# Optimization experiments

Measured on AMD Instinct MI355X. Metric: run time of the kernel, lower is better.

## Reference

```python
import jax, jax.numpy as jnp
import numpy as np

B, T, D, H = 256, 256, 384, 64  # batch, seq (BLOCK_SIZE), D_MODEL, HEAD_SIZE


def setup_inputs() -> dict:
    key = jax.random.key(0)
    k1, k2, k3, k4 = jax.random.split(key, 4)
    x = jax.random.normal(k1, (B, T, D), dtype=jnp.float32)
    # nn.Linear(D, H, bias=False): weight [H, D]; we store transposed [D, H] for x @ W
    Wq = jax.random.normal(k2, (D, H), dtype=jnp.float32) * (1.0 / np.sqrt(D))
    Wk = jax.random.normal(k3, (D, H), dtype=jnp.float32) * (1.0 / np.sqrt(D))
    Wv = jax.random.normal(k4, (D, H), dtype=jnp.float32) * (1.0 / np.sqrt(D))
    return {"x": x, "Wq": Wq, "Wk": Wk, "Wv": Wv}


def reference(x, Wq, Wk, Wv):
    # x: [B, T, D]
    q = x @ Wq  # [B, T, H]
    k = x @ Wk  # [B, T, H]
    v = x @ Wv  # [B, T, H]
    scale = 1.0 / jnp.sqrt(jnp.asarray(k.shape[-1], dtype=x.dtype))
    wei = jnp.einsum('bth,bsh->bts', q, k) * scale  # [B, T, T]
    causal = jnp.tril(jnp.ones((x.shape[1], x.shape[1]), dtype=bool))
    wei = jnp.where(causal, wei, -jnp.inf)
    wei = jax.nn.softmax(wei, axis=-1)
    # dropout is identity in eval mode (deterministic reference)
    out = jnp.einsum('bts,bsh->bth', wei, v)  # [B, T, H]
    return out
```

## Files before the change

### kernel.cpp

```cpp
#include <hip/hip_runtime.h>

#define BATCH 256
#define TT 256
#define DD 384
#define HH 64
#define SCALE 0.125f
#define SHIFT 14.0f

typedef __attribute__((ext_vector_type(8))) short short8;
typedef __attribute__((ext_vector_type(4))) float floatx4;

#define KS_STRIDE 72
#define QS_STRIDE 72
#define VT_STRIDE 264
#define PS_STRIDE 40

__device__ __forceinline__ unsigned short f2bf(float f) {
    unsigned int u = __float_as_uint(f);
    u += 0x7fffu + ((u >> 16) & 1u);
    return (unsigned short)(u >> 16);
}
__device__ __forceinline__ float bf2f(unsigned short u) {
    return __uint_as_float(((unsigned int)u) << 16);
}

__device__ __forceinline__ void gld_lds16(const float* g, float* ldst) {
    __builtin_amdgcn_global_load_lds(
        (__attribute__((address_space(1))) void*)(unsigned long long)(const void*)g,
        (__attribute__((address_space(3))) void*)(unsigned int)(unsigned long long)(void*)ldst,
        16, 0, 0);
}

__global__ void pack_w_kernel(const float* __restrict__ wq,
                              const float* __restrict__ wk,
                              const float* __restrict__ wv,
                              unsigned short* __restrict__ wf) {
    int idx = blockIdx.x * 256 + threadIdx.x;
    if (idx >= 3 * DD * HH) return;
    int j = idx & 7;
    int lane = (idx >> 3) & 63;
    int nt = (idx >> 9) & 3;
    int rem = idx >> 11;
    int mat = rem % 3;
    int ch = rem / 3;
    int l16 = lane & 15, q = lane >> 4;
    int h = 16 * nt + l16;
    int d = 32 * ch + 8 * q + j;
    const float* w = (mat == 0) ? wq : (mat == 1) ? wk : wv;
    wf[idx] = f2bf(w[d * HH + h]);
}

__device__ __forceinline__ short8 afrag(const float* xsbuf, int row, int quad) {
    int r7 = row & 7;
    float4 f0 = *(const float4*)(xsbuf + row * 32 + ((2 * quad) ^ r7) * 4);
    float4 f1 = *(const float4*)(xsbuf + row * 32 + ((2 * quad + 1) ^ r7) * 4);
    short8 a;
    a[0] = (short)f2bf(f0.x); a[1] = (short)f2bf(f0.y);
    a[2] = (short)f2bf(f0.z); a[3] = (short)f2bf(f0.w);
    a[4] = (short)f2bf(f1.x); a[5] = (short)f2bf(f1.y);
    a[6] = (short)f2bf(f1.z); a[7] = (short)f2bf(f1.w);
    return a;
}

__global__ __launch_bounds__(512, 2)
void fused_kernel(const float* __restrict__ x, const unsigned short* __restrict__ wfrag,
                  float* __restrict__ out) {
    __shared__ __align__(16) unsigned short Ks[TT * KS_STRIDE];
    __shared__ __align__(16) unsigned short Vt[HH * VT_STRIDE];
    __shared__ __align__(16) union StageU {
        float xs[2][TT * 32];
        struct {
            unsigned short q[TT * QS_STRIDE];
            unsigned short p[8][16 * PS_STRIDE];
        } s;
    } U;

    const int b = blockIdx.x;
    const int tid = threadIdx.x;
    const int wave = tid >> 6;
    const int lane = tid & 63;
    const int quad = lane >> 4;
    const int l16 = lane & 15;

    const float* xb = x + (size_t)b * TT * DD;

    floatx4 cq[2][4] = {};
    floatx4 ck[2][4] = {};
    floatx4 cv[2][4] = {};

    #define STAGE_X(buf_, kk_)                                                    \
        {                                                                         \
            _Pragma("unroll")                                                     \
            for (int rr = 0; rr < 4; ++rr) {                                      \
                int u = rr * 512 + wave * 64 + lane;                              \
                int row_ = u >> 3;                                                \
                int slot_ = (u & 7) ^ (row_ & 7);                                 \
                gld_lds16(xb + row_ * DD + (kk_) + slot_ * 4,                     \
                          U.xs[buf_] + (rr * 512 + wave * 64) * 4);               \
            }                                                                     \
        }

    short8 wf[12], wfn[12];
    #pragma unroll
    for (int i = 0; i < 12; ++i)
        wf[i] = *(const short8*)(wfrag + (size_t)i * 512 + lane * 8);
    STAGE_X(0, 0);

    for (int ch = 0; ch < 12; ++ch) {
        __syncthreads();
        if (ch + 1 < 12) {
            #pragma unroll
            for (int i = 0; i < 12; ++i)
                wfn[i] = *(const short8*)(wfrag + (size_t)((ch + 1) * 12 + i) * 512 + lane * 8);
            STAGE_X((ch + 1) & 1, (ch + 1) * 32);
        }
        const float* xsb = U.xs[ch & 1];
        short8 a0 = afrag(xsb, 32 * wave + l16, quad);
        short8 a1 = afrag(xsb, 32 * wave + 16 + l16, quad);
        #pragma unroll
        for (int nt = 0; nt < 4; ++nt) {
            cq[0][nt] = __builtin_amdgcn_mfma_f32_16x16x32_bf16(a0, wf[nt], cq[0][nt], 0, 0, 0);
            cq[1][nt] = __builtin_amdgcn_mfma_f32_16x16x32_bf16(a1, wf[nt], cq[1][nt], 0, 0, 0);
            ck[0][nt] = __builtin_amdgcn_mfma_f32_16x16x32_bf16(a0, wf[4 + nt], ck[0][nt], 0, 0, 0);
            ck[1][nt] = __builtin_amdgcn_mfma_f32_16x16x32_bf16(a1, wf[4 + nt], ck[1][nt], 0, 0, 0);
            cv[0][nt] = __builtin_amdgcn_mfma_f32_16x16x32_bf16(a0, wf[8 + nt], cv[0][nt], 0, 0, 0);
            cv[1][nt] = __builtin_amdgcn_mfma_f32_16x16x32_bf16(a1, wf[8 + nt], cv[1][nt], 0, 0, 0);
        }
        #pragma unroll
        for (int i = 0; i < 12; ++i) wf[i] = wfn[i];
    }

    __syncthreads();

    #pragma unroll
    for (int mi = 0; mi < 2; ++mi)
      #pragma unroll
      for (int nt = 0; nt < 4; ++nt)
        #pragma unroll
        for (int r = 0; r < 4; ++r) {
            int row = 32 * wave + 16 * mi + 4 * quad + r;
            int col = 16 * nt + l16;
            U.s.q[row * QS_STRIDE + col] = f2bf(cq[mi][nt][r]);
            Ks[row * KS_STRIDE + col] = f2bf(ck[mi][nt][r]);
            Vt[col * VT_STRIDE + row] = f2bf(cv[mi][nt][r]);
        }

    __syncthreads();

    floatx4 o[2][4] = {};
    float l_run[2][4] = {{0.f, 0.f, 0.f, 0.f}, {0.f, 0.f, 0.f, 0.f}};
    unsigned short* psw = U.s.p[wave];

    #pragma unroll
    for (int gi = 0; gi < 2; ++gi) {
        int g = gi ? (15 - wave) : wave;
        int gr0 = 16 * g;
        short8 aq0 = *(const short8*)(U.s.q + (gr0 + l16) * QS_STRIDE + quad * 8);
        short8 aq1 = *(const short8*)(U.s.q + (gr0 + l16) * QS_STRIDE + 32 + quad * 8);
        int clast = g >> 1;
        for (int c = 0; c <= clast; ++c) {
            floatx4 s[2] = {};
            #pragma unroll
            for (int ni = 0; ni < 2; ++ni) {
                const unsigned short* kbase =
                    Ks + (size_t)(32 * c + 16 * ni + l16) * KS_STRIDE + quad * 8;
                s[ni] = __builtin_amdgcn_mfma_f32_16x16x32_bf16(aq0, *(const short8*)(kbase), s[ni], 0, 0, 0);
                s[ni] = __builtin_amdgcn_mfma_f32_16x16x32_bf16(aq1, *(const short8*)(kbase + 32), s[ni], 0, 0, 0);
            }
            bool partial = (c == clast);
            #pragma unroll
            for (int r = 0; r < 4; ++r) {
                int row = gr0 + 4 * quad + r;
                float p0 = __expf(s[0][r] * SCALE - SHIFT);
                float p1 = __expf(s[1][r] * SCALE - SHIFT);
                if (partial) {
                    if (32 * c + l16 > row) p0 = 0.f;
                    if (32 * c + 16 + l16 > row) p1 = 0.f;
                }
                unsigned short b0 = f2bf(p0), b1 = f2bf(p1);
                l_run[gi][r] += bf2f(b0) + bf2f(b1);
                psw[(4 * quad + r) * PS_STRIDE + l16] = b0;
                psw[(4 * quad + r) * PS_STRIDE + 16 + l16] = b1;
            }
            short8 ap = *(const short8*)(psw + l16 * PS_STRIDE + quad * 8);
            #pragma unroll
            for (int nt = 0; nt < 4; ++nt) {
                short8 bv = *(const short8*)(Vt + (size_t)(16 * nt + l16) * VT_STRIDE + 32 * c + quad * 8);
                o[gi][nt] = __builtin_amdgcn_mfma_f32_16x16x32_bf16(ap, bv, o[gi][nt], 0, 0, 0);
            }
        }
    }

    float* outb = out + (size_t)b * TT * HH;
    #pragma unroll
    for (int gi = 0; gi < 2; ++gi) {
        int g = gi ? (15 - wave) : wave;
        #pragma unroll
        for (int r = 0; r < 4; ++r) {
            float l = l_run[gi][r];
            l += __shfl_xor(l, 1);
            l += __shfl_xor(l, 2);
            l += __shfl_xor(l, 4);
            l += __shfl_xor(l, 8);
            l_run[gi][r] = l;
        }
        #pragma unroll
        for (int nt = 0; nt < 4; ++nt)
          #pragma unroll
          for (int r = 0; r < 4; ++r) {
            int row = 16 * g + 4 * quad + r;
            outb[(size_t)row * HH + 16 * nt + l16] = o[gi][nt][r] / l_run[gi][r];
          }
    }
}

extern "C" void kernel_launch(void* const* d_in, const int* in_sizes, int n_in,
                              void* d_out, int out_size, void* d_ws, size_t ws_size,
                              hipStream_t stream) {
    const float* x  = (const float*)d_in[0];
    const float* wq = (const float*)d_in[1];
    const float* wk = (const float*)d_in[2];
    const float* wv = (const float*)d_in[3];
    unsigned short* wf = (unsigned short*)d_ws;
    float* o = (float*)d_out;

    pack_w_kernel<<<(3 * DD * HH + 255) / 256, 256, 0, stream>>>(wq, wk, wv, wf);
    fused_kernel<<<BATCH, 512, 0, stream>>>(x, wf, o);
}
```

Baseline: 168.8 us.

## Stage packed weights in LDS once and stream x directly into registers

All bf16 weight fragments (144 KB) are copied into LDS once at block start, replacing the per-chunk global reloads of weights. The x chunks are now loaded straight from global into registers with a register double-buffer, instead of going through LDS staging with a barrier every chunk. This removes 12 barriers and repeated weight traffic from the projection loop. The cost is more LDS per block (the union now holds 144 KB), which may limit occupancy to one block per CU despite launch_bounds(512,2). It also uses uncoalesced row-strided x loads from global memory.

```diff
diff --git a/kernel.cpp b/kernel.cpp
--- a/kernel.cpp
+++ b/kernel.cpp
@@ -14,6 +14,7 @@
 #define QS_STRIDE 72
 #define VT_STRIDE 264
 #define PS_STRIDE 40
+#define WELEMS (3 * DD * HH)
 
 __device__ __forceinline__ unsigned short f2bf(float f) {
     unsigned int u = __float_as_uint(f);
@@ -24,11 +25,20 @@
     return __uint_as_float(((unsigned int)u) << 16);
 }
 
-__device__ __forceinline__ void gld_lds16(const float* g, float* ldst) {
+__device__ __forceinline__ void gld_lds16(const void* g, void* ldst) {
     __builtin_amdgcn_global_load_lds(
-        (__attribute__((address_space(1))) void*)(unsigned long long)(const void*)g,
-        (__attribute__((address_space(3))) void*)(unsigned int)(unsigned long long)(void*)ldst,
+        (__attribute__((address_space(1))) void*)(unsigned long long)g,
+        (__attribute__((address_space(3))) void*)(unsigned int)(unsigned long long)ldst,
         16, 0, 0);
+}
+
+__device__ __forceinline__ short8 cvt8(float4 f0, float4 f1) {
+    short8 a;
+    a[0] = (short)f2bf(f0.x); a[1] = (short)f2bf(f0.y);
+    a[2] = (short)f2bf(f0.z); a[3] = (short)f2bf(f0.w);
+    a[4] = (short)f2bf(f1.x); a[5] = (short)f2bf(f1.y);
+    a[6] = (short)f2bf(f1.z); a[7] = (short)f2bf(f1.w);
+    return a;
 }
 
 __global__ void pack_w_kernel(const float* __restrict__ wq,
@@ -36,7 +46,7 @@
                               const float* __restrict__ wv,
                               unsigned short* __restrict__ wf) {
     int idx = blockIdx.x * 256 + threadIdx.x;
-    if (idx >= 3 * DD * HH) return;
+    if (idx >= WELEMS) return;
     int j = idx & 7;
     int lane = (idx >> 3) & 63;
     int nt = (idx >> 9) & 3;
@@ -50,26 +60,14 @@
     wf[idx] = f2bf(w[d * HH + h]);
 }
 
-__device__ __forceinline__ short8 afrag(const float* xsbuf, int row, int quad) {
-    int r7 = row & 7;
-    float4 f0 = *(const float4*)(xsbuf + row * 32 + ((2 * quad) ^ r7) * 4);
-    float4 f1 = *(const float4*)(xsbuf + row * 32 + ((2 * quad + 1) ^ r7) * 4);
-    short8 a;
-    a[0] = (short)f2bf(f0.x); a[1] = (short)f2bf(f0.y);
-    a[2] = (short)f2bf(f0.z); a[3] = (short)f2bf(f0.w);
-    a[4] = (short)f2bf(f1.x); a[5] = (short)f2bf(f1.y);
-    a[6] = (short)f2bf(f1.z); a[7] = (short)f2bf(f1.w);
-    return a;
-}
-
 __global__ __launch_bounds__(512, 2)
 void fused_kernel(const float* __restrict__ x, const unsigned short* __restrict__ wfrag,
                   float* __restrict__ out) {
-    __shared__ __align__(16) unsigned short Ks[TT * KS_STRIDE];
-    __shared__ __align__(16) unsigned short Vt[HH * VT_STRIDE];
-    __shared__ __align__(16) union StageU {
-        float xs[2][TT * 32];
+    __shared__ __align__(16) union LdsU {
+        unsigned short w[WELEMS];
         struct {
+            unsigned short ks[TT * KS_STRIDE];
+            unsigned short vt[HH * VT_STRIDE];
             unsigned short q[TT * QS_STRIDE];
             unsigned short p[8][16 * PS_STRIDE];
         } s;
@@ -84,51 +82,61 @@
 
     const float* xb = x + (size_t)b * TT * DD;
 
+    const float* xr0 = xb + (size_t)(32 * wave + l16) * DD + 8 * quad;
+    const float* xr1 = xr0 + (size_t)16 * DD;
+
     floatx4 cq[2][4] = {};
     floatx4 ck[2][4] = {};
     floatx4 cv[2][4] = {};
 
-    #define STAGE_X(buf_, kk_)                                                    \
-        {                                                                         \
-            _Pragma("unroll")                                                     \
-            for (int rr = 0; rr < 4; ++rr) {                                      \
-                int u = rr * 512 + wave * 64 + lane;                              \
-                int row_ = u >> 3;                                                \
-                int slot_ = (u & 7) ^ (row_ & 7);                                 \
-                gld_lds16(xb + row_ * DD + (kk_) + slot_ * 4,                     \
-                          U.xs[buf_] + (rr * 512 + wave * 64) * 4);               \
-            }                                                                     \
-        }
-
-    short8 wf[12], wfn[12];
-    #pragma unroll
-    for (int i = 0; i < 12; ++i)
-        wf[i] = *(const short8*)(wfrag + (size_t)i * 512 + lane * 8);
-    STAGE_X(0, 0);
-
-    for (int ch = 0; ch < 12; ++ch) {
-        __syncthreads();
-        if (ch + 1 < 12) {
-            #pragma unroll
-            for (int i = 0; i < 12; ++i)
-                wfn[i] = *(const short8*)(wfrag + (size_t)((ch + 1) * 12 + i) * 512 + lane * 8);
-            STAGE_X((ch + 1) & 1, (ch + 1) * 32);
-        }
-        const float* xsb = U.xs[ch & 1];
-        short8 a0 = afrag(xsb, 32 * wave + l16, quad);
-        short8 a1 = afrag(xsb, 32 * wave + 16 + l16, quad);
-        #pragma unroll
-        for (int nt = 0; nt < 4; ++nt) {
-            cq[0][nt] = __builtin_amdgcn_mfma_f32_16x16x32_bf16(a0, wf[nt], cq[0][nt], 0, 0, 0);
-            cq[1][nt] = __builtin_amdgcn_mfma_f32_16x16x32_bf16(a1, wf[nt], cq[1][nt], 0, 0, 0);
-            ck[0][nt] = __builtin_amdgcn_mfma_f32_16x16x32_bf16(a0, wf[4 + nt], ck[0][nt], 0, 0, 0);
-            ck[1][nt] = __builtin_amdgcn_mfma_f32_16x16x32_bf16(a1, wf[4 + nt], ck[1][nt], 0, 0, 0);
-            cv[0][nt] = __builtin_amdgcn_mfma_f32_16x16x32_bf16(a0, wf[8 + nt], cv[0][nt], 0, 0, 0);
-            cv[1][nt] = __builtin_amdgcn_mfma_f32_16x16x32_bf16(a1, wf[8 + nt], cv[1][nt], 0, 0, 0);
-        }
-        #pragma unroll
-        for (int i = 0; i < 12; ++i) wf[i] = wfn[i];
-    }
+    float4 xfA[4], xfB[4];
+
+    xfA[0] = *(const float4*)(xr0);
+    xfA[1] = *(const float4*)(xr0 + 4);
+    xfA[2] = *(const float4*)(xr1);
+    xfA[3] = *(const float4*)(xr1 + 4);
+
+    #pragma unroll
+    for (int t = 0; t < 18; ++t) {
+        int grp = wave * 18 + t;
+        gld_lds16(wfrag + (size_t)grp * 512 + lane * 8, U.w + grp * 512);
+    }
+
+    __syncthreads();
+
+    #define GEMM_BODY(CUR, NXT, CH, PREF)                                          \
+        {                                                                          \
+            if (PREF) {                                                            \
+                const float* p0_ = xr0 + ((CH) + 1) * 32;                          \
+                const float* p1_ = xr1 + ((CH) + 1) * 32;                          \
+                NXT[0] = *(const float4*)(p0_);                                    \
+                NXT[1] = *(const float4*)(p0_ + 4);                                \
+                NXT[2] = *(const float4*)(p1_);                                    \
+                NXT[3] = *(const float4*)(p1_ + 4);                                \
+            }                                                                      \
+            short8 wf_[12];                                                        \
+            _Pragma("unroll")                                                      \
+            for (int i = 0; i < 12; ++i)                                           \
+                wf_[i] = *(const short8*)(U.w + (size_t)((CH) * 12 + i) * 512 + lane * 8); \
+            short8 a0 = cvt8(CUR[0], CUR[1]);                                      \
+            short8 a1 = cvt8(CUR[2], CUR[3]);                                      \
+            _Pragma("unroll")                                                      \
+            for (int nt = 0; nt < 4; ++nt) {                                       \
+                cq[0][nt] = __builtin_amdgcn_mfma_f32_16x16x32_bf16(a0, wf_[nt], cq[0][nt], 0, 0, 0);      \
+                cq[1][nt] = __builtin_amdgcn_mfma_f32_16x16x32_bf16(a1, wf_[nt], cq[1][nt], 0, 0, 0);      \
+                ck[0][nt] = __builtin_amdgcn_mfma_f32_16x16x32_bf16(a0, wf_[4 + nt], ck[0][nt], 0, 0, 0);  \
+                ck[1][nt] = __builtin_amdgcn_mfma_f32_16x16x32_bf16(a1, wf_[4 + nt], ck[1][nt], 0, 0, 0);  \
+                cv[0][nt] = __builtin_amdgcn_mfma_f32_16x16x32_bf16(a0, wf_[8 + nt], cv[0][nt], 0, 0, 0);  \
+                cv[1][nt] = __builtin_amdgcn_mfma_f32_16x16x32_bf16(a1, wf_[8 + nt], cv[1][nt], 0, 0, 0);  \
+            }                                                                      \
+        }
+
+    #pragma unroll 1
+    for (int t = 0; t < 6; ++t) {
+        GEMM_BODY(xfA, xfB, 2 * t, 1);
+        GEMM_BODY(xfB, xfA, 2 * t + 1, (t < 5));
+    }
+    #undef GEMM_BODY
 
     __syncthreads();
 
@@ -141,8 +149,8 @@
             int row = 32 * wave + 16 * mi + 4 * quad + r;
             int col = 16 * nt + l16;
             U.s.q[row * QS_STRIDE + col] = f2bf(cq[mi][nt][r]);
-            Ks[row * KS_STRIDE + col] = f2bf(ck[mi][nt][r]);
-            Vt[col * VT_STRIDE + row] = f2bf(cv[mi][nt][r]);
+            U.s.ks[row * KS_STRIDE + col] = f2bf(ck[mi][nt][r]);
+            U.s.vt[col * VT_STRIDE + row] = f2bf(cv[mi][nt][r]);
         }
 
     __syncthreads();
@@ -155,15 +163,15 @@
     for (int gi = 0; gi < 2; ++gi) {
         int g = gi ? (15 - wave) : wave;
         int gr0 = 16 * g;
-        short8 aq0 = *(const short8*)(U.s.q + (gr0 + l16) * QS_STRIDE + quad * 8);
-        short8 aq1 = *(const short8*)(U.s.q + (gr0 + l16) * QS_STRIDE + 32 + quad * 8);
+        short8 aq0 = *(const short8*)(U.s.q + (size_t)(gr0 + l16) * QS_STRIDE + quad * 8);
+        short8 aq1 = *(const short8*)(U.s.q + (size_t)(gr0 + l16) * QS_STRIDE + 32 + quad * 8);
         int clast = g >> 1;
         for (int c = 0; c <= clast; ++c) {
             floatx4 s[2] = {};
             #pragma unroll
             for (int ni = 0; ni < 2; ++ni) {
                 const unsigned short* kbase =
-                    Ks + (size_t)(32 * c + 16 * ni + l16) * KS_STRIDE + quad * 8;
+                    U.s.ks + (size_t)(32 * c + 16 * ni + l16) * KS_STRIDE + quad * 8;
                 s[ni] = __builtin_amdgcn_mfma_f32_16x16x32_bf16(aq0, *(const short8*)(kbase), s[ni], 0, 0, 0);
                 s[ni] = __builtin_amdgcn_mfma_f32_16x16x32_bf16(aq1, *(const short8*)(kbase + 32), s[ni], 0, 0, 0);
             }
@@ -185,7 +193,7 @@
             short8 ap = *(const short8*)(psw + l16 * PS_STRIDE + quad * 8);
             #pragma unroll
             for (int nt = 0; nt < 4; ++nt) {
-                short8 bv = *(const short8*)(Vt + (size_t)(16 * nt + l16) * VT_STRIDE + 32 * c + quad * 8);
+                short8 bv = *(const short8*)(U.s.vt + (size_t)(16 * nt + l16) * VT_STRIDE + 32 * c + quad * 8);
                 o[gi][nt] = __builtin_amdgcn_mfma_f32_16x16x32_bf16(ap, bv, o[gi][nt], 0, 0, 0);
             }
         }
@@ -224,6 +232,6 @@
     unsigned short* wf = (unsigned short*)d_ws;
     float* o = (float*)d_out;
 
-    pack_w_kernel<<<(3 * DD * HH + 255) / 256, 256, 0, stream>>>(wq, wk, wv, wf);
+    pack_w_kernel<<<(WELEMS + 255) / 256, 256, 0, stream>>>(wq, wk, wv, wf);
     fused_kernel<<<BATCH, 512, 0, stream>>>(x, wf, o);
 }
```

After: 169.1 us. No clear change (+0.2%).
